# Kernel tuning notes

Hardware: AMD Instinct MI355X
Metric: run time of the kernel (lower is better)

Reference implementation:

```python
import jax, jax.numpy as jnp
import numpy as np

N_USERS = 100000
N_ITEMS = 50000
DIM = 64
HID = 64
E = 3200000
B = 16384


def setup_inputs() -> dict:
    key = jax.random.key(0)
    ks = jax.random.split(key, 16)
    N = N_USERS + N_ITEMS
    return {
        "users": jax.random.randint(ks[0], (B,), 0, N_USERS),
        "items": jax.random.randint(ks[1], (B,), 0, N_ITEMS),
        "edge_index": jax.random.randint(ks[2], (2, E), 0, N),
        "edge_weight": jax.random.uniform(ks[3], (E,), dtype=jnp.float32),
        # learned parameters
        "U": jax.random.normal(ks[4], (N_USERS, DIM), jnp.float32) * 0.1,
        "I": jax.random.normal(ks[5], (N_ITEMS, DIM), jnp.float32) * 0.1,
        "W0": jax.random.normal(ks[6], (DIM, HID), jnp.float32) / np.sqrt(DIM),
        "b0": jnp.zeros((HID,), jnp.float32),
        "g0": jnp.ones((HID,), jnp.float32),
        "be0": jnp.zeros((HID,), jnp.float32),
        "W1": jax.random.normal(ks[7], (HID, HID), jnp.float32) / np.sqrt(HID),
        "b1": jnp.zeros((HID,), jnp.float32),
        "g1": jnp.ones((HID,), jnp.float32),
        "be1": jnp.zeros((HID,), jnp.float32),
        "Wp": jax.random.normal(ks[8], (HID, DIM), jnp.float32) / np.sqrt(HID),
        "bp": jnp.zeros((DIM,), jnp.float32),
        "bu": jnp.zeros((N_USERS,), jnp.float32),
        "bi": jnp.zeros((N_ITEMS,), jnp.float32),
        "mu": jnp.zeros((), jnp.float32),
    }


def _layernorm(h, g, b, eps=1e-5):
    m = jnp.mean(h, axis=-1, keepdims=True)
    v = jnp.mean(jnp.square(h - m), axis=-1, keepdims=True)
    return (h - m) * jax.lax.rsqrt(v + eps) * g + b


def reference(users, items, edge_index, edge_weight, U, I,
              W0, b0, g0, be0, W1, b1, g1, be1, Wp, bp, bu, bi, mu):
    N = U.shape[0] + I.shape[0]
    x = jnp.concatenate([U, I], axis=0)  # [N, DIM]

    # GCN normalization with added self-loops (torch_geometric gcn_norm)
    loop = jnp.arange(N)
    src = jnp.concatenate([edge_index[0], loop])
    dst = jnp.concatenate([edge_index[1], loop])
    ew = jnp.concatenate([edge_weight, jnp.ones((N,), edge_weight.dtype)])
    deg = jax.ops.segment_sum(ew, dst, num_segments=N)
    dinv = jnp.where(deg > 0, jax.lax.rsqrt(deg), 0.0)
    norm = dinv[src] * ew * dinv[dst]  # [E+N]

    def conv(h, W, b):
        hw = h @ W  # [N, HID]
        msgs = norm[:, None] * hw[src]  # gather: [E+N, HID]
        return jax.ops.segment_sum(msgs, dst, num_segments=N) + b

    # layer 0: conv -> layernorm -> relu -> (dropout=identity, eval) -> residual
    h = x
    h_in = h
    h = conv(h, W0, b0)
    h = jax.nn.relu(_layernorm(h, g0, be0)) + h_in
    # layer 1
    h_in = h
    h = conv(h, W1, b1)
    h = jax.nn.relu(_layernorm(h, g1, be1)) + h_in

    h = h @ Wp + bp  # proj_out: [N, DIM]
    h_user = h[:U.shape[0]]
    h_item = h[U.shape[0]:]

    s = jnp.sum(h_user[users] * h_item[items], axis=-1)
    s = s + bu[users] + bi[items] + mu
    return jnp.clip(s, 1.0, 5.0)
```

## Files before the change

kernel.cpp:

```cpp
#include <hip/hip_runtime.h>

#define NU 100000
#define NI 50000
#define NN 150000
#define D  64
#define CAP 47
#define OVF_MAX 4096

#define BINSHIFT 8
#define BINW 256
#define NBINS 586
#define BINCAP 5848
#define STAGE_CAP 11
#define EPT 4
#define SPILL_CAP 262144
#define BIN_BLOCKS 768

typedef unsigned int uint;
typedef unsigned short ushort;
typedef unsigned char uchar;

__device__ __forceinline__ float half_reduce_add(float v) {
    #pragma unroll
    for (int m = 16; m >= 1; m >>= 1) v += __shfl_xor(v, m, 64);
    return v;
}
__device__ __forceinline__ ushort f2bf(float f) {
    union { float f; uint i; } c; c.f = f;
    uint r = c.i + 0x7FFF + ((c.i >> 16) & 1);
    return (ushort)(r >> 16);
}
__device__ __forceinline__ float lane_bcast(float v, int l) {
    return __int_as_float(__builtin_amdgcn_readlane(__float_as_int(v), l));
}
__device__ __forceinline__ uint enc14(float w) {
    uint b = __float_as_uint(w) + 0x00020000u;
    return b & 0xFFFC0000u;
}
__device__ __forceinline__ float dec14(uint r) {
    return __uint_as_float(r & 0xFFFC0000u);
}
__device__ __forceinline__ void spill_one(int d, uint s, float w,
        uint2* __restrict__ spill, int* __restrict__ spillcnt) {
    int si = atomicAdd(spillcnt, 1);
    if (si < SPILL_CAP) spill[si] = make_uint2(s | enc14(w), (uint)d);
}

__global__ __launch_bounds__(256) void k_bin(
        const int* __restrict__ src, const int* __restrict__ dst,
        const float* __restrict__ ew, int* __restrict__ bincur,
        uint2* __restrict__ binbuf, uint2* __restrict__ spill,
        int* __restrict__ spillcnt, uint2* __restrict__ tail,
        uchar* __restrict__ cnt8, int E) {
    __shared__ uint2 stage[NBINS][STAGE_CAP];
    __shared__ int scnt[NBINS];
    int t = threadIdx.x;
    for (int i = t; i < NBINS; i += 256) scnt[i] = 0;
    __syncthreads();
    const int batch = 256 * EPT;
    for (int base = blockIdx.x * batch; base < E; base += BIN_BLOCKS * batch) {
        int dd[EPT]; uint ss[EPT]; float ww[EPT]; int ok[EPT];
        #pragma unroll
        for (int k = 0; k < EPT; ++k) {
            int e = base + k * 256 + t;
            ok[k] = (e < E);
            if (ok[k]) { dd[k] = dst[e]; ss[k] = (uint)src[e]; ww[k] = ew[e]; }
        }
        #pragma unroll
        for (int k = 0; k < EPT; ++k) {
            if (!ok[k]) continue;
            int bin = dd[k] >> BINSHIFT;
            int slot = atomicAdd(&scnt[bin], 1);
            if (slot < STAGE_CAP) {
                stage[bin][slot] = make_uint2(
                    ss[k] | ((uint)(dd[k] & (BINW - 1)) << 18),
                    (uint)__float_as_int(ww[k]));
            } else {
                spill_one(dd[k], ss[k], ww[k], spill, spillcnt);
            }
        }
        __syncthreads();
        for (int bin = t; bin < NBINS; bin += 256) {
            int c = scnt[bin]; if (c > STAGE_CAP) c = STAGE_CAP;
            while (c >= 8) {
                int b0 = atomicAdd(&bincur[bin], 8);
                if (b0 + 8 <= BINCAP) {
                    uint4* o4 = (uint4*)(binbuf + (size_t)bin * BINCAP + b0);
                    uint2* s2 = &stage[bin][c - 8];
                    o4[0] = make_uint4(s2[0].x, s2[0].y, s2[1].x, s2[1].y);
                    o4[1] = make_uint4(s2[2].x, s2[2].y, s2[3].x, s2[3].y);
                    o4[2] = make_uint4(s2[4].x, s2[4].y, s2[5].x, s2[5].y);
                    o4[3] = make_uint4(s2[6].x, s2[6].y, s2[7].x, s2[7].y);
                } else {
                    for (int j = 0; j < 8; ++j) {
                        uint2 r = stage[bin][c - 8 + j];
                        spill_one((bin << BINSHIFT) + (int)(r.x >> 18),
                                  r.x & 0x3FFFFu, __int_as_float((int)r.y),
                                  spill, spillcnt);
                    }
                }
                c -= 8;
            }
            scnt[bin] = c;
        }
        __syncthreads();
    }
    uchar* cb = cnt8 + (size_t)blockIdx.x * NBINS;
    for (int i = t; i < NBINS; i += 256) cb[i] = (uchar)scnt[i];
    uint2* tb = tail + (size_t)blockIdx.x * (NBINS * 8);
    for (int i = t; i < NBINS * 8; i += 256) tb[i] = stage[i >> 3][i & 7];
}

__global__ __launch_bounds__(256) void k_regroup(
        const int* __restrict__ bincur, const uint2* __restrict__ binbuf,
        const uint2* __restrict__ spill, const int* __restrict__ spillcnt,
        const uint2* __restrict__ tail, const uchar* __restrict__ cnt8,
        uint* __restrict__ recs, int* __restrict__ cursor,
        float* __restrict__ dinv, int4* __restrict__ ovf,
        int* __restrict__ ovfcnt) {
    __shared__ uint image[256 * CAP];
    __shared__ int cnt[256];
    __shared__ float ovfw[256];
    int t = threadIdx.x;
    int bin = blockIdx.x;
    cnt[t] = 0; ovfw[t] = 0.0f;
    __syncthreads();
    int dbase = bin << BINSHIFT;
    int nrec = bincur[bin]; if (nrec > BINCAP) nrec = BINCAP;
    const uint2* bb = binbuf + (size_t)bin * BINCAP;
    for (int i = t; i < nrec; i += 256) {
        uint2 r = bb[i];
        int dl = (int)(r.x >> 18);
        int slot = atomicAdd(&cnt[dl], 1);
        uint s = r.x & 0x3FFFFu;
        float w = __int_as_float((int)r.y);
        if (slot < CAP) image[dl * CAP + slot] = enc14(w) | s;
        else {
            atomicAdd(&ovfw[dl], w);
            int o = atomicAdd(ovfcnt, 1);
            if (o < OVF_MAX)
                ovf[o] = make_int4(dbase + dl, (int)s, __float_as_int(w), 0);
        }
    }
    for (int g = t; g < BIN_BLOCKS; g += 256) {
        int c = cnt8[(size_t)g * NBINS + bin];
        const uint2* tb = tail + ((size_t)g * NBINS + bin) * 8;
        for (int j = 0; j < c; ++j) {
            uint2 r = tb[j];
            int dl = (int)(r.x >> 18);
            int slot = atomicAdd(&cnt[dl], 1);
            uint s = r.x & 0x3FFFFu;
            float w = __int_as_float((int)r.y);
            if (slot < CAP) image[dl * CAP + slot] = enc14(w) | s;
            else {
                atomicAdd(&ovfw[dl], w);
                int o = atomicAdd(ovfcnt, 1);
                if (o < OVF_MAX)
                    ovf[o] = make_int4(dbase + dl, (int)s, __float_as_int(w), 0);
            }
        }
    }
    int ns = spillcnt[0]; if (ns > SPILL_CAP) ns = SPILL_CAP;
    for (int i = t; i < ns; i += 256) {
        uint2 e = spill[i];
        int d = (int)e.y;
        if (d < dbase || d >= dbase + BINW) continue;
        int dl = d - dbase;
        int slot = atomicAdd(&cnt[dl], 1);
        if (slot < CAP) image[dl * CAP + slot] = e.x;
        else {
            float w = dec14(e.x);
            atomicAdd(&ovfw[dl], w);
            int o = atomicAdd(ovfcnt, 1);
            if (o < OVF_MAX) ovf[o] = make_int4(d, (int)(e.x & 0x3FFFFu),
                                                __float_as_int(w), 0);
        }
    }
    __syncthreads();
    int ndl = NN - dbase; if (ndl > 256) ndl = 256;
    if (ndl <= 0) return;
    if (t < ndl) {
        int c = cnt[t];
        cursor[dbase + t] = c;
        if (c > CAP) c = CAP;
        float dg = ovfw[t];
        for (int j = 0; j < c; ++j) dg += dec14(image[t * CAP + j]);
        dinv[dbase + t] = rsqrtf(dg + 1.0f);
    }
    int tot = ndl * CAP;
    uint* out = recs + (size_t)dbase * CAP;
    for (int i = t; i < tot; i += 256) out[i] = image[i];
}

__global__ __launch_bounds__(256) void k_gemm1(
        const float* __restrict__ U, const float* __restrict__ I,
        const float* __restrict__ W, const float* __restrict__ dinv,
        ushort* __restrict__ out) {
    int lane = threadIdx.x & 63;
    float wreg[64];
    #pragma unroll
    for (int k = 0; k < 64; ++k) wreg[k] = W[k * 64 + lane];
    int wpb = blockDim.x >> 6;
    int wid = blockIdx.x * wpb + (threadIdx.x >> 6);
    int tw = gridDim.x * wpb;
    for (int n = wid; n < NN; n += tw) {
        float xv = (n < NU) ? U[(size_t)n * D + lane]
                            : I[(size_t)(n - NU) * D + lane];
        float a0 = 0.f, a1 = 0.f, a2 = 0.f, a3 = 0.f;
        #pragma unroll
        for (int k = 0; k < 64; k += 4) {
            a0 = fmaf(lane_bcast(xv, k + 0), wreg[k + 0], a0);
            a1 = fmaf(lane_bcast(xv, k + 1), wreg[k + 1], a1);
            a2 = fmaf(lane_bcast(xv, k + 2), wreg[k + 2], a2);
            a3 = fmaf(lane_bcast(xv, k + 3), wreg[k + 3], a3);
        }
        out[(size_t)n * D + lane] = f2bf(((a0 + a1) + (a2 + a3)) * dinv[n]);
    }
}

#define CA_DECL(c) uint x##c##0, x##c##1, x##c##2, x##c##3, \
                        w##c##0, w##c##1, w##c##2, w##c##3;
#define CA_GET(c, i, P, rvv) { \
    uint r = (uint)__builtin_amdgcn_ds_bpermute(vodd4 + 8 * (P), (int)(rvv)); \
    w##c##i = r & 0xFFFC0000u; \
    x##c##i = *(const uint*)((const char*)hw2p + \
                             (((r & 0x3FFFFu) << 7) + lb4)); }
#define CA_ISSUE(c, P0, rvv) { CA_GET(c, 0, (P0)+0, rvv) CA_GET(c, 1, (P0)+1, rvv) \
                               CA_GET(c, 2, (P0)+2, rvv) CA_GET(c, 3, (P0)+3, rvv) }
#define CA_FMA1(c, i, axv, ayv) { \
    axv = fmaf(__uint_as_float(w##c##i), __uint_as_float(x##c##i << 16), axv); \
    ayv = fmaf(__uint_as_float(w##c##i), \
               __uint_as_float(x##c##i & 0xFFFF0000u), ayv); }
#define CA_FMA(c, axv, ayv) { CA_FMA1(c,0,axv,ayv) CA_FMA1(c,1,axv,ayv) \
                              CA_FMA1(c,2,axv,ayv) CA_FMA1(c,3,axv,ayv) }

__device__ __forceinline__ float2 conv_accum2(int n, int lane,
        const uint* __restrict__ hw2p, const int* __restrict__ cursor,
        const uint* __restrict__ recs, const int4* __restrict__ ovf,
        const int* __restrict__ ovfcnt) {
    int cnt = __builtin_amdgcn_readfirstlane(cursor[n]);
    if (cnt > CAP) cnt = CAP;
    uint rv = (lane < cnt) ? recs[(size_t)n * CAP + lane] : 0u;
    const int  vodd4 = (lane >> 5) << 2;
    const uint lb4   = (uint)(lane & 31) << 2;
    uint xs = *(const uint*)((const char*)hw2p + (((uint)n << 7) + lb4));
    float ax = 0.f, ay = 0.f;
    int cp = (cnt + 7) & ~7;
    CA_DECL(A) CA_DECL(B) CA_DECL(G)
    CA_ISSUE(A, 0, rv) CA_ISSUE(B, 4, rv) CA_ISSUE(G, 8, rv)
    CA_FMA(A, ax, ay)
    if (cp > 24) CA_ISSUE(A, 12, rv)
    CA_FMA(B, ax, ay)
    if (cp > 32) CA_ISSUE(B, 16, rv)
    CA_FMA(G, ax, ay)
    if (cp > 40) CA_ISSUE(G, 20, rv)
    if (cp > 24) CA_FMA(A, ax, ay)
    if (cp > 32) CA_FMA(B, ax, ay)
    if (cp > 40) CA_FMA(G, ax, ay)
    ax += __shfl_xor(ax, 32, 64);
    ay += __shfl_xor(ay, 32, 64);
    ax += __uint_as_float(xs << 16);
    ay += __uint_as_float(xs & 0xFFFF0000u);
    int novf = __builtin_amdgcn_readfirstlane(ovfcnt[0]);
    if (novf > 0) {
        if (novf > OVF_MAX) novf = OVF_MAX;
        for (int j = 0; j < novf; ++j) {
            int4 e = ovf[j];
            if (e.x == n) {
                float w = __int_as_float(e.z);
                uint x = hw2p[(size_t)e.y * 32 + (lane & 31)];
                ax = fmaf(w, __int_as_float((int)(x << 16)), ax);
                ay = fmaf(w, __int_as_float((int)(x & 0xFFFF0000u)), ay);
            }
        }
    }
    return make_float2(ax, ay);
}

#define CB_DECL(p, c) uint p##x##c##0, p##x##c##1, p##x##c##2, p##x##c##3, \
                           p##w##c##0, p##w##c##1, p##w##c##2, p##w##c##3;
#define CB_GET(p, c, i, P, rvv) { \
    uint r = (uint)__builtin_amdgcn_ds_bpermute(vodd4 + 8 * (P), (int)(rvv)); \
    p##w##c##i = r & 0xFFFC0000u; \
    p##x##c##i = *(const uint*)((const char*)hw2p + \
                                (((r & 0x3FFFFu) << 7) + lb4)); }
#define CB_ISSUE(p, c, P0, rvv) { CB_GET(p,c,0,(P0)+0,rvv) CB_GET(p,c,1,(P0)+1,rvv) \
                                  CB_GET(p,c,2,(P0)+2,rvv) CB_GET(p,c,3,(P0)+3,rvv) }
#define CB_FMA1(p, c, i, axv, ayv) { \
    axv = fmaf(__uint_as_float(p##w##c##i), \
               __uint_as_float(p##x##c##i << 16), axv); \
    ayv = fmaf(__uint_as_float(p##w##c##i), \
               __uint_as_float(p##x##c##i & 0xFFFF0000u), ayv); }
#define CB_FMA(p, c, axv, ayv) { CB_FMA1(p,c,0,axv,ayv) CB_FMA1(p,c,1,axv,ayv) \
                                 CB_FMA1(p,c,2,axv,ayv) CB_FMA1(p,c,3,axv,ayv) }

__device__ __forceinline__ void conv_accum2_dual(int nu, int ni, int lane,
        const uint* __restrict__ hw2p, const int* __restrict__ cursor,
        const uint* __restrict__ recs, const int4* __restrict__ ovf,
        const int* __restrict__ ovfcnt, float2* outu, float2* outi) {
    int cu = __builtin_amdgcn_readfirstlane(cursor[nu]); if (cu > CAP) cu = CAP;
    int ci = __builtin_amdgcn_readfirstlane(cursor[ni]); if (ci > CAP) ci = CAP;
    uint rvu = (lane < cu) ? recs[(size_t)nu * CAP + lane] : 0u;
    uint rvi = (lane < ci) ? recs[(size_t)ni * CAP + lane] : 0u;
    const int  vodd4 = (lane >> 5) << 2;
    const uint lb4   = (uint)(lane & 31) << 2;
    uint xsu = *(const uint*)((const char*)hw2p + (((uint)nu << 7) + lb4));
    uint xsi = *(const uint*)((const char*)hw2p + (((uint)ni << 7) + lb4));
    float uax = 0.f, uay = 0.f, iax = 0.f, iay = 0.f;
    int cpu_ = (cu + 7) & ~7, cpi_ = (ci + 7) & ~7;
    CB_DECL(u, A) CB_DECL(u, B) CB_DECL(u, G)
    CB_DECL(i, A) CB_DECL(i, B) CB_DECL(i, G)
    CB_ISSUE(u, A, 0, rvu) CB_ISSUE(i, A, 0, rvi)
    CB_ISSUE(u, B, 4, rvu) CB_ISSUE(i, B, 4, rvi)
    CB_ISSUE(u, G, 8, rvu) CB_ISSUE(i, G, 8, rvi)
    CB_FMA(u, A, uax, uay) CB_FMA(i, A, iax, iay)
    if (cpu_ > 24) CB_ISSUE(u, A, 12, rvu)
    if (cpi_ > 24) CB_ISSUE(i, A, 12, rvi)
    CB_FMA(u, B, uax, uay) CB_FMA(i, B, iax, iay)
    if (cpu_ > 32) CB_ISSUE(u, B, 16, rvu)
    if (cpi_ > 32) CB_ISSUE(i, B, 16, rvi)
    CB_FMA(u, G, uax, uay) CB_FMA(i, G, iax, iay)
    if (cpu_ > 40) CB_ISSUE(u, G, 20, rvu)
    if (cpi_ > 40) CB_ISSUE(i, G, 20, rvi)
    if (cpu_ > 24) CB_FMA(u, A, uax, uay)
    if (cpi_ > 24) CB_FMA(i, A, iax, iay)
    if (cpu_ > 32) CB_FMA(u, B, uax, uay)
    if (cpi_ > 32) CB_FMA(i, B, iax, iay)
    if (cpu_ > 40) CB_FMA(u, G, uax, uay)
    if (cpi_ > 40) CB_FMA(i, G, iax, iay)
    uax += __shfl_xor(uax, 32, 64); uay += __shfl_xor(uay, 32, 64);
    iax += __shfl_xor(iax, 32, 64); iay += __shfl_xor(iay, 32, 64);
    uax += __uint_as_float(xsu << 16); uay += __uint_as_float(xsu & 0xFFFF0000u);
    iax += __uint_as_float(xsi << 16); iay += __uint_as_float(xsi & 0xFFFF0000u);
    int novf = __builtin_amdgcn_readfirstlane(ovfcnt[0]);
    if (novf > 0) {
        if (novf > OVF_MAX) novf = OVF_MAX;
        for (int j = 0; j < novf; ++j) {
            int4 e = ovf[j];
            if (e.x == nu || e.x == ni) {
                float w = __int_as_float(e.z);
                uint x = hw2p[(size_t)e.y * 32 + (lane & 31)];
                float fx = __uint_as_float(x << 16);
                float fy = __uint_as_float(x & 0xFFFF0000u);
                if (e.x == nu) { uax = fmaf(w, fx, uax); uay = fmaf(w, fy, uay); }
                else           { iax = fmaf(w, fx, iax); iay = fmaf(w, fy, iay); }
            }
        }
    }
    *outu = make_float2(uax, uay);
    *outi = make_float2(iax, iay);
}

__device__ __forceinline__ float2 ln_relu2(float2 a, float di, int p,
        const float* __restrict__ b, const float* __restrict__ g,
        const float* __restrict__ be) {
    float2 bb = ((const float2*)b)[p];
    float v0 = fmaf(a.x, di, bb.x);
    float v1 = fmaf(a.y, di, bb.y);
    float m = half_reduce_add(v0 + v1) * (1.0f / 64.0f);
    float d0 = v0 - m, d1 = v1 - m;
    float var = half_reduce_add(d0 * d0 + d1 * d1) * (1.0f / 64.0f);
    float rs = rsqrtf(var + 1e-5f);
    float2 gg = ((const float2*)g)[p];
    float2 ee = ((const float2*)be)[p];
    return make_float2(fmaxf(fmaf(d0 * rs, gg.x, ee.x), 0.0f),
                       fmaxf(fmaf(d1 * rs, gg.y, ee.y), 0.0f));
}

__global__ __launch_bounds__(256) void k_conv1(
        const uint* __restrict__ hw2p, const int* __restrict__ cursor,
        const uint* __restrict__ recs, const int4* __restrict__ ovf,
        const int* __restrict__ ovfcnt, const float* __restrict__ dinv,
        const float* __restrict__ b, const float* __restrict__ g,
        const float* __restrict__ be, const float* __restrict__ U,
        const float* __restrict__ I, uint* __restrict__ out1) {
    int lane = threadIdx.x & 63;
    int n = __builtin_amdgcn_readfirstlane(blockIdx.x * 4 + (threadIdx.x >> 6));
    if (n >= NN) return;
    float2 a = conv_accum2(n, lane, hw2p, cursor, recs, ovf, ovfcnt);
    int p = lane & 31;
    float2 y = ln_relu2(a, dinv[n], p, b, g, be);
    const float* R = (n < NU) ? (U + (size_t)n * D) : (I + (size_t)(n - NU) * D);
    float2 rr = ((const float2*)R)[p];
    if (lane < 32) {
        out1[(size_t)n * 32 + p] =
            (uint)f2bf(y.x + rr.x) | ((uint)f2bf(y.y + rr.y) << 16);
    }
}

__global__ __launch_bounds__(256) void k_gemm2(
        const ushort* __restrict__ hb, const float* __restrict__ W,
        const float* __restrict__ dinv, ushort* __restrict__ out) {
    int lane = threadIdx.x & 63;
    float wreg[64];
    #pragma unroll
    for (int k = 0; k < 64; ++k) wreg[k] = W[k * 64 + lane];
    int wpb = blockDim.x >> 6;
    int wid = blockIdx.x * wpb + (threadIdx.x >> 6);
    int tw = gridDim.x * wpb;
    for (int n = wid; n < NN; n += tw) {
        float xv = __uint_as_float((uint)hb[(size_t)n * D + lane] << 16);
        float a0 = 0.f, a1 = 0.f, a2 = 0.f, a3 = 0.f;
        #pragma unroll
        for (int k = 0; k < 64; k += 4) {
            a0 = fmaf(lane_bcast(xv, k + 0), wreg[k + 0], a0);
            a1 = fmaf(lane_bcast(xv, k + 1), wreg[k + 1], a1);
            a2 = fmaf(lane_bcast(xv, k + 2), wreg[k + 2], a2);
            a3 = fmaf(lane_bcast(xv, k + 3), wreg[k + 3], a3);
        }
        out[(size_t)n * D + lane] = f2bf(((a0 + a1) + (a2 + a3)) * dinv[n]);
    }
}

__global__ __launch_bounds__(256) void k_conv2score(
        const uint* __restrict__ hw2p, const int* __restrict__ cursor,
        const uint* __restrict__ recs, const int4* __restrict__ ovf,
        const int* __restrict__ ovfcnt, const float* __restrict__ dinv,
        const float* __restrict__ b, const float* __restrict__ g,
        const float* __restrict__ be, const int* __restrict__ users,
        const int* __restrict__ items, const uint* __restrict__ h1b,
        const float* __restrict__ Wp, const float* __restrict__ bp,
        const float* __restrict__ bu, const float* __restrict__ bi,
        const float* __restrict__ mu, float* __restrict__ out, int B) {
    __shared__ float wlds[64 * 64];
    int t = threadIdx.x;
    for (int i = t; i < 64 * 64; i += 256) wlds[i] = Wp[i];
    __syncthreads();
    int lane = t & 63;
    float bpl = bp[lane];
    int q = lane & 31;
    int wpb = blockDim.x >> 6;
    int wid = blockIdx.x * wpb + (t >> 6);
    int tw = gridDim.x * wpb;
    for (int p = wid; p < B; p += tw) {
        int un = users[p];
        int in_ = NU + items[p];
        int nu = __builtin_amdgcn_readfirstlane(un);
        int ni = __builtin_amdgcn_readfirstlane(in_);
        float2 au, ai;
        conv_accum2_dual(nu, ni, lane, hw2p, cursor, recs, ovf, ovfcnt,
                         &au, &ai);
        float2 yu = ln_relu2(au, dinv[nu], q, b, g, be);
        float2 yi = ln_relu2(ai, dinv[ni], q, b, g, be);
        uint xu = h1b[(size_t)nu * 32 + q];
        uint xi = h1b[(size_t)ni * 32 + q];
        float2 hu = make_float2(yu.x + __uint_as_float(xu << 16),
                                yu.y + __uint_as_float(xu & 0xFFFF0000u));
        float2 hi = make_float2(yi.x + __uint_as_float(xi << 16),
                                yi.y + __uint_as_float(xi & 0xFFFF0000u));
        float pu = bpl, pi = bpl;
        #pragma unroll
        for (int j = 0; j < 32; ++j) {
            float w0 = wlds[(2 * j) * 64 + lane];
            float w1 = wlds[(2 * j + 1) * 64 + lane];
            pu = fmaf(lane_bcast(hu.x, j), w0, pu);
            pu = fmaf(lane_bcast(hu.y, j), w1, pu);
            pi = fmaf(lane_bcast(hi.x, j), w0, pi);
            pi = fmaf(lane_bcast(hi.y, j), w1, pi);
        }
        float dot = pu * pi;
        #pragma unroll
        for (int m = 32; m >= 1; m >>= 1) dot += __shfl_xor(dot, m, 64);
        if (lane == 0) {
            dot += bu[un] + bi[in_ - NU] + mu[0];
            out[p] = fminf(fmaxf(dot, 1.0f), 5.0f);
        }
    }
}

extern "C" void kernel_launch(void* const* d_in, const int* in_sizes, int n_in,
                              void* d_out, int out_size, void* d_ws, size_t ws_size,
                              hipStream_t stream) {
    const int*   users = (const int*)d_in[0];
    const int*   items = (const int*)d_in[1];
    const int*   ei2   = (const int*)d_in[2];
    const float* ew    = (const float*)d_in[3];
    const float* U     = (const float*)d_in[4];
    const float* I     = (const float*)d_in[5];
    const float* W0    = (const float*)d_in[6];
    const float* b0    = (const float*)d_in[7];
    const float* g0    = (const float*)d_in[8];
    const float* be0   = (const float*)d_in[9];
    const float* W1    = (const float*)d_in[10];
    const float* b1    = (const float*)d_in[11];
    const float* g1    = (const float*)d_in[12];
    const float* be1   = (const float*)d_in[13];
    const float* Wp    = (const float*)d_in[14];
    const float* bp    = (const float*)d_in[15];
    const float* bu    = (const float*)d_in[16];
    const float* bi    = (const float*)d_in[17];
    const float* mu    = (const float*)d_in[18];

    int B = in_sizes[0];
    int E = in_sizes[2] / 2;
    const int* srcp = ei2;
    const int* dstp = ei2 + E;

    char* p = (char*)d_ws;
    auto alloc = [&](size_t bytes) -> char* {
        char* r = p;
        p += (bytes + 255) & ~(size_t)255;
        return r;
    };
    int*    cbuf    = (int*)  alloc((size_t)(NBINS + 8) * 4);
    int*    bincur  = cbuf;
    int*    spillcnt= cbuf + NBINS;
    int*    ovfcnt  = cbuf + NBINS + 1;
    int*    cursor  = (int*)  alloc((size_t)NN * 4);
    float*  dinv    = (float*)alloc((size_t)NN * 4);
    int4*   ovf     = (int4*) alloc((size_t)OVF_MAX * 16);
    uint2*  spill   = (uint2*)alloc((size_t)SPILL_CAP * 8);
    uchar*  cnt8    = (uchar*)alloc((size_t)BIN_BLOCKS * NBINS);
    uint2*  binbuf  = (uint2*)alloc((size_t)NBINS * BINCAP * 8);
    uint*   recs    = (uint*) alloc((size_t)NN * CAP * 4);
    ushort* hw2b    = (ushort*)alloc((size_t)NN * D * 2);
    uint*   h1b     = (uint*) alloc((size_t)NN * 32 * 4);
    const uint* hw2p = (const uint*)hw2b;
    uint2*  tail    = (uint2*)hw2b;

    hipMemsetAsync(cbuf, 0, (size_t)(NBINS + 8) * 4, stream);

    int gW = (NN + 3) / 4;

    k_bin<<<BIN_BLOCKS, 256, 0, stream>>>(srcp, dstp, ew, bincur, binbuf,
                                          spill, spillcnt, tail, cnt8, E);
    k_regroup<<<NBINS, 256, 0, stream>>>(bincur, binbuf, spill, spillcnt,
                                         tail, cnt8, recs, cursor, dinv,
                                         ovf, ovfcnt);

    k_gemm1<<<2048, 256, 0, stream>>>(U, I, W0, dinv, hw2b);
    k_conv1<<<gW, 256, 0, stream>>>(hw2p, cursor, recs, ovf, ovfcnt, dinv,
                                    b0, g0, be0, U, I, h1b);
    k_gemm2<<<2048, 256, 0, stream>>>((const ushort*)h1b, W1, dinv, hw2b);
    k_conv2score<<<2048, 256, 0, stream>>>(hw2p, cursor, recs, ovf, ovfcnt, dinv,
                                           b1, g1, be1, users, items, h1b,
                                           Wp, bp, bu, bi, mu,
                                           (float*)d_out, B);
}
```

Measured before the change: 419.0 us.

## Pad bin counters to separate cache lines and widen conv1 gathers to 8 bytes

Each per-bin atomic counter now sits in its own 64-byte slot, so atomics from different bins no longer contend on the same cache lines. k_conv1 is rewritten so 16 lanes cover a 64-wide row with 8-byte loads, and four edges are processed per wave step instead of two. LayerNorm is redone with 16-lane reductions. This cuts the number of gather instructions and widens each memory access, at the cost of extra cross-lane reductions and a larger counter memset.

```diff
diff --git a/kernel.cpp b/kernel.cpp
--- a/kernel.cpp
+++ b/kernel.cpp
@@ -15,6 +15,7 @@
 #define EPT 4
 #define SPILL_CAP 262144
 #define BIN_BLOCKS 768
+#define BCPAD 16
 
 typedef unsigned int uint;
 typedef unsigned short ushort;
@@ -23,6 +24,11 @@
 __device__ __forceinline__ float half_reduce_add(float v) {
     #pragma unroll
     for (int m = 16; m >= 1; m >>= 1) v += __shfl_xor(v, m, 64);
+    return v;
+}
+__device__ __forceinline__ float quad_reduce_add(float v) {
+    #pragma unroll
+    for (int m = 8; m >= 1; m >>= 1) v += __shfl_xor(v, m, 64);
     return v;
 }
 __device__ __forceinline__ ushort f2bf(float f) {
@@ -83,7 +89,7 @@
         for (int bin = t; bin < NBINS; bin += 256) {
             int c = scnt[bin]; if (c > STAGE_CAP) c = STAGE_CAP;
             while (c >= 8) {
-                int b0 = atomicAdd(&bincur[bin], 8);
+                int b0 = atomicAdd(&bincur[bin * BCPAD], 8);
                 if (b0 + 8 <= BINCAP) {
                     uint4* o4 = (uint4*)(binbuf + (size_t)bin * BINCAP + b0);
                     uint2* s2 = &stage[bin][c - 8];
@@ -126,7 +132,7 @@
     cnt[t] = 0; ovfw[t] = 0.0f;
     __syncthreads();
     int dbase = bin << BINSHIFT;
-    int nrec = bincur[bin]; if (nrec > BINCAP) nrec = BINCAP;
+    int nrec = bincur[bin * BCPAD]; if (nrec > BINCAP) nrec = BINCAP;
     const uint2* bb = binbuf + (size_t)bin * BINCAP;
     for (int i = t; i < nrec; i += 256) {
         uint2 r = bb[i];
@@ -218,49 +224,58 @@
     }
 }
 
-#define CA_DECL(c) uint x##c##0, x##c##1, x##c##2, x##c##3, \
-                        w##c##0, w##c##1, w##c##2, w##c##3;
-#define CA_GET(c, i, P, rvv) { \
-    uint r = (uint)__builtin_amdgcn_ds_bpermute(vodd4 + 8 * (P), (int)(rvv)); \
+#define CQ_DECL(c) uint2 x##c##0, x##c##1; uint w##c##0, w##c##1;
+#define CQ_GET(c, i, P, rvv) { \
+    uint r = (uint)__builtin_amdgcn_ds_bpermute(vg4 + 4 * (P), (int)(rvv)); \
     w##c##i = r & 0xFFFC0000u; \
-    x##c##i = *(const uint*)((const char*)hw2p + \
-                             (((r & 0x3FFFFu) << 7) + lb4)); }
-#define CA_ISSUE(c, P0, rvv) { CA_GET(c, 0, (P0)+0, rvv) CA_GET(c, 1, (P0)+1, rvv) \
-                               CA_GET(c, 2, (P0)+2, rvv) CA_GET(c, 3, (P0)+3, rvv) }
-#define CA_FMA1(c, i, axv, ayv) { \
-    axv = fmaf(__uint_as_float(w##c##i), __uint_as_float(x##c##i << 16), axv); \
-    ayv = fmaf(__uint_as_float(w##c##i), \
-               __uint_as_float(x##c##i & 0xFFFF0000u), ayv); }
-#define CA_FMA(c, axv, ayv) { CA_FMA1(c,0,axv,ayv) CA_FMA1(c,1,axv,ayv) \
-                              CA_FMA1(c,2,axv,ayv) CA_FMA1(c,3,axv,ayv) }
-
-__device__ __forceinline__ float2 conv_accum2(int n, int lane,
+    x##c##i = *(const uint2*)((const char*)hw2p + \
+                              (((r & 0x3FFFFu) << 7) + lb8)); }
+#define CQ_ISSUE(c, P0, rvv) { CQ_GET(c, 0, (P0), rvv) CQ_GET(c, 1, (P0)+4, rvv) }
+#define CQ_FMA1(c, i) { \
+    float wf = __uint_as_float(w##c##i); \
+    ax = fmaf(wf, __uint_as_float(x##c##i.x << 16), ax); \
+    ay = fmaf(wf, __uint_as_float(x##c##i.x & 0xFFFF0000u), ay); \
+    az = fmaf(wf, __uint_as_float(x##c##i.y << 16), az); \
+    aw = fmaf(wf, __uint_as_float(x##c##i.y & 0xFFFF0000u), aw); }
+#define CQ_FMA(c) { CQ_FMA1(c, 0) CQ_FMA1(c, 1) }
+
+__global__ __launch_bounds__(256) void k_conv1(
         const uint* __restrict__ hw2p, const int* __restrict__ cursor,
         const uint* __restrict__ recs, const int4* __restrict__ ovf,
-        const int* __restrict__ ovfcnt) {
+        const int* __restrict__ ovfcnt, const float* __restrict__ dinv,
+        const float* __restrict__ b, const float* __restrict__ g,
+        const float* __restrict__ be, const float* __restrict__ U,
+        const float* __restrict__ I, uint* __restrict__ out1) {
+    int lane = threadIdx.x & 63;
+    int n = __builtin_amdgcn_readfirstlane(blockIdx.x * 4 + (threadIdx.x >> 6));
+    if (n >= NN) return;
     int cnt = __builtin_amdgcn_readfirstlane(cursor[n]);
     if (cnt > CAP) cnt = CAP;
     uint rv = (lane < cnt) ? recs[(size_t)n * CAP + lane] : 0u;
-    const int  vodd4 = (lane >> 5) << 2;
-    const uint lb4   = (uint)(lane & 31) << 2;
-    uint xs = *(const uint*)((const char*)hw2p + (((uint)n << 7) + lb4));
-    float ax = 0.f, ay = 0.f;
+    const int  vg4 = (lane >> 4) << 2;
+    const uint lb8 = (uint)(lane & 15) << 3;
+    uint2 xs = *(const uint2*)((const char*)hw2p + (((uint)n << 7) + lb8));
+    float ax = 0.f, ay = 0.f, az = 0.f, aw = 0.f;
     int cp = (cnt + 7) & ~7;
-    CA_DECL(A) CA_DECL(B) CA_DECL(G)
-    CA_ISSUE(A, 0, rv) CA_ISSUE(B, 4, rv) CA_ISSUE(G, 8, rv)
-    CA_FMA(A, ax, ay)
-    if (cp > 24) CA_ISSUE(A, 12, rv)
-    CA_FMA(B, ax, ay)
-    if (cp > 32) CA_ISSUE(B, 16, rv)
-    CA_FMA(G, ax, ay)
-    if (cp > 40) CA_ISSUE(G, 20, rv)
-    if (cp > 24) CA_FMA(A, ax, ay)
-    if (cp > 32) CA_FMA(B, ax, ay)
-    if (cp > 40) CA_FMA(G, ax, ay)
-    ax += __shfl_xor(ax, 32, 64);
-    ay += __shfl_xor(ay, 32, 64);
-    ax += __uint_as_float(xs << 16);
-    ay += __uint_as_float(xs & 0xFFFF0000u);
+    CQ_DECL(A) CQ_DECL(B) CQ_DECL(G)
+    CQ_ISSUE(A, 0, rv) CQ_ISSUE(B, 8, rv) CQ_ISSUE(G, 16, rv)
+    CQ_FMA(A)
+    if (cp > 24) CQ_ISSUE(A, 24, rv)
+    CQ_FMA(B)
+    if (cp > 32) CQ_ISSUE(B, 32, rv)
+    CQ_FMA(G)
+    if (cp > 40) CQ_ISSUE(G, 40, rv)
+    if (cp > 24) CQ_FMA(A)
+    if (cp > 32) CQ_FMA(B)
+    if (cp > 40) CQ_FMA(G)
+    ax += __shfl_xor(ax, 32, 64); ax += __shfl_xor(ax, 16, 64);
+    ay += __shfl_xor(ay, 32, 64); ay += __shfl_xor(ay, 16, 64);
+    az += __shfl_xor(az, 32, 64); az += __shfl_xor(az, 16, 64);
+    aw += __shfl_xor(aw, 32, 64); aw += __shfl_xor(aw, 16, 64);
+    ax += __uint_as_float(xs.x << 16);
+    ay += __uint_as_float(xs.x & 0xFFFF0000u);
+    az += __uint_as_float(xs.y << 16);
+    aw += __uint_as_float(xs.y & 0xFFFF0000u);
     int novf = __builtin_amdgcn_readfirstlane(ovfcnt[0]);
     if (novf > 0) {
         if (novf > OVF_MAX) novf = OVF_MAX;
@@ -268,13 +283,40 @@
             int4 e = ovf[j];
             if (e.x == n) {
                 float w = __int_as_float(e.z);
-                uint x = hw2p[(size_t)e.y * 32 + (lane & 31)];
-                ax = fmaf(w, __int_as_float((int)(x << 16)), ax);
-                ay = fmaf(w, __int_as_float((int)(x & 0xFFFF0000u)), ay);
+                uint2 x = *(const uint2*)((const char*)hw2p +
+                                          (((uint)e.y << 7) + lb8));
+                ax = fmaf(w, __uint_as_float(x.x << 16), ax);
+                ay = fmaf(w, __uint_as_float(x.x & 0xFFFF0000u), ay);
+                az = fmaf(w, __uint_as_float(x.y << 16), az);
+                aw = fmaf(w, __uint_as_float(x.y & 0xFFFF0000u), aw);
             }
         }
     }
-    return make_float2(ax, ay);
+    int q = lane & 15;
+    float di = dinv[n];
+    float4 bb = ((const float4*)b)[q];
+    float v0 = fmaf(ax, di, bb.x);
+    float v1 = fmaf(ay, di, bb.y);
+    float v2 = fmaf(az, di, bb.z);
+    float v3 = fmaf(aw, di, bb.w);
+    float m = quad_reduce_add((v0 + v1) + (v2 + v3)) * (1.0f / 64.0f);
+    float d0 = v0 - m, d1 = v1 - m, d2 = v2 - m, d3 = v3 - m;
+    float var = quad_reduce_add((d0 * d0 + d1 * d1) + (d2 * d2 + d3 * d3))
+                * (1.0f / 64.0f);
+    float rs = rsqrtf(var + 1e-5f);
+    float4 gg = ((const float4*)g)[q];
+    float4 ee = ((const float4*)be)[q];
+    float y0 = fmaxf(fmaf(d0 * rs, gg.x, ee.x), 0.0f);
+    float y1 = fmaxf(fmaf(d1 * rs, gg.y, ee.y), 0.0f);
+    float y2 = fmaxf(fmaf(d2 * rs, gg.z, ee.z), 0.0f);
+    float y3 = fmaxf(fmaf(d3 * rs, gg.w, ee.w), 0.0f);
+    const float* R = (n < NU) ? (U + (size_t)n * D) : (I + (size_t)(n - NU) * D);
+    float4 rr = ((const float4*)R)[q];
+    if (lane < 16) {
+        uint lo = (uint)f2bf(y0 + rr.x) | ((uint)f2bf(y1 + rr.y) << 16);
+        uint hi = (uint)f2bf(y2 + rr.z) | ((uint)f2bf(y3 + rr.w) << 16);
+        ((uint2*)out1)[(size_t)n * 16 + q] = make_uint2(lo, hi);
+    }
 }
 
 #define CB_DECL(p, c) uint p##x##c##0, p##x##c##1, p##x##c##2, p##x##c##3, \
@@ -367,27 +409,6 @@
                        fmaxf(fmaf(d1 * rs, gg.y, ee.y), 0.0f));
 }
 
-__global__ __launch_bounds__(256) void k_conv1(
-        const uint* __restrict__ hw2p, const int* __restrict__ cursor,
-        const uint* __restrict__ recs, const int4* __restrict__ ovf,
-        const int* __restrict__ ovfcnt, const float* __restrict__ dinv,
-        const float* __restrict__ b, const float* __restrict__ g,
-        const float* __restrict__ be, const float* __restrict__ U,
-        const float* __restrict__ I, uint* __restrict__ out1) {
-    int lane = threadIdx.x & 63;
-    int n = __builtin_amdgcn_readfirstlane(blockIdx.x * 4 + (threadIdx.x >> 6));
-    if (n >= NN) return;
-    float2 a = conv_accum2(n, lane, hw2p, cursor, recs, ovf, ovfcnt);
-    int p = lane & 31;
-    float2 y = ln_relu2(a, dinv[n], p, b, g, be);
-    const float* R = (n < NU) ? (U + (size_t)n * D) : (I + (size_t)(n - NU) * D);
-    float2 rr = ((const float2*)R)[p];
-    if (lane < 32) {
-        out1[(size_t)n * 32 + p] =
-            (uint)f2bf(y.x + rr.x) | ((uint)f2bf(y.y + rr.y) << 16);
-    }
-}
-
 __global__ __launch_bounds__(256) void k_gemm2(
         const ushort* __restrict__ hb, const float* __restrict__ W,
         const float* __restrict__ dinv, ushort* __restrict__ out) {
@@ -502,10 +523,10 @@
         p += (bytes + 255) & ~(size_t)255;
         return r;
     };
-    int*    cbuf    = (int*)  alloc((size_t)(NBINS + 8) * 4);
+    int*    cbuf    = (int*)  alloc((size_t)(NBINS * BCPAD + 32) * 4);
     int*    bincur  = cbuf;
-    int*    spillcnt= cbuf + NBINS;
-    int*    ovfcnt  = cbuf + NBINS + 1;
+    int*    spillcnt= cbuf + NBINS * BCPAD;
+    int*    ovfcnt  = cbuf + NBINS * BCPAD + 16;
     int*    cursor  = (int*)  alloc((size_t)NN * 4);
     float*  dinv    = (float*)alloc((size_t)NN * 4);
     int4*   ovf     = (int4*) alloc((size_t)OVF_MAX * 16);
@@ -518,7 +539,7 @@
     const uint* hw2p = (const uint*)hw2b;
     uint2*  tail    = (uint2*)hw2b;
 
-    hipMemsetAsync(cbuf, 0, (size_t)(NBINS + 8) * 4, stream);
+    hipMemsetAsync(cbuf, 0, (size_t)(NBINS * BCPAD + 32) * 4, stream);
 
     int gW = (NN + 3) / 4;
 
```

Measured after the change: 403.0 us. 1.04x faster.
